# Optimization experiments

Measured on AMD Instinct MI355X. Metric: run time of the kernel, lower is better.

The kernel has to match this reference:

```python
import jax, jax.numpy as jnp
import numpy as np

N, MEM_SIZE, MEM_DIM = 65536, 2048, 256

def setup_inputs() -> dict:
    key = jax.random.key(0)
    k1, k2 = jax.random.split(key)
    x = jax.random.normal(k1, (N, MEM_DIM), dtype=jnp.float32)
    # xavier_uniform for memory parameter [memory_size, memory_dim]
    limit = np.sqrt(6.0 / (MEM_SIZE + MEM_DIM)).astype(np.float32)
    memory = jax.random.uniform(k2, (MEM_SIZE, MEM_DIM), dtype=jnp.float32,
                                minval=-limit, maxval=limit)
    return {"x": x, "memory": memory}

def reference(x, memory):
    # scores: [N, memory_size] = x @ memory^T (unscaled)
    scores = jnp.einsum('nd,md->nm', x, memory)
    attention_weights = jax.nn.softmax(scores, axis=-1)
    memory_output = jnp.einsum('nm,md->nd', attention_weights, memory)
    return (memory_output, attention_weights)
```

## Files before the change

kernel.cpp:

```cpp
#include <hip/hip_runtime.h>
#include <hip/hip_bf16.h>
#include <stdint.h>

#define NQ 65536
#define MM 2048
#define DD 256

typedef __bf16 bf16x8 __attribute__((ext_vector_type(8)));
typedef float f32x16 __attribute__((ext_vector_type(16)));
typedef unsigned short u16;
typedef unsigned int u32;
typedef u16 u16x8 __attribute__((ext_vector_type(8)));

typedef __attribute__((address_space(3))) u32 lds_u32;
typedef __attribute__((address_space(1))) u32 glb_u32;

#define GLOAD16(gsrc, ldst)                                                    \
  __builtin_amdgcn_global_load_lds((glb_u32*)(uintptr_t)(gsrc),                \
                                   (lds_u32*)(u32)(uintptr_t)(ldst), 16, 0, 0)

__device__ __forceinline__ u16 f32_to_bf16_rtne(float v) {
  u32 u = __builtin_bit_cast(u32, v);
  u += 0x7FFFu + ((u >> 16) & 1u);
  return (u16)(u >> 16);
}

__global__ __launch_bounds__(256) void mem_convert_kernel(
    const float* __restrict__ memory, u16* __restrict__ memb,
    u16* __restrict__ memTswz) {
  int tid = blockIdx.x * 256 + threadIdx.x;
  u16 b = f32_to_bf16_rtne(memory[tid]);
  memb[tid] = b;
  int m = tid >> 8, d = tid & 255;
  int t = m >> 5, mi = m & 31;
  int c = mi >> 3, e = mi & 7;
  int slot = c ^ ((d >> 1) & 3);
  memTswz[(size_t)t * 8192 + (size_t)(d * 4 + slot) * 8 + e] = b;
}


__global__ __launch_bounds__(256, 2) void pass1_kernel(
    const float* __restrict__ x, const u16* __restrict__ memb,
    u16* __restrict__ p_e, float* __restrict__ sums) {
  __shared__ __align__(16) char stage[2][32768];
  __shared__ __align__(16) u16 plds[4][32][40];

  const int tid = threadIdx.x;
  const int wv = tid >> 6;
  const int l = tid & 63;
  const int q5 = l & 31;
  const int h = l >> 5;
  const int qw = blockIdx.x * 128 + wv * 32;
  const int qt = blockIdx.x * 4 + wv;

  bf16x8 aq[16];
  {
    const float* xrow = x + (size_t)(qw + q5) * DD;
#pragma unroll
    for (int ks = 0; ks < 16; ++ks) {
      const float4 f0 = *(const float4*)(xrow + ks * 16 + h * 8);
      const float4 f1 = *(const float4*)(xrow + ks * 16 + h * 8 + 4);
      bf16x8 a;
      a[0] = (__bf16)f0.x; a[1] = (__bf16)f0.y;
      a[2] = (__bf16)f0.z; a[3] = (__bf16)f0.w;
      a[4] = (__bf16)f1.x; a[5] = (__bf16)f1.y;
      a[6] = (__bf16)f1.z; a[7] = (__bf16)f1.w;
      aq[ks] = a;
    }
  }

  auto STAGE1 = [&](int mt, char* buf) {
#pragma unroll
    for (int i = 0; i < 8; ++i) {
      const int wc = wv * 8 + i;
      const int row = wc * 2 + h;
      const int csrc = q5 ^ (row & 7);
      GLOAD16(memb + (((size_t)(mt * 64 + row)) << 8) + csrc * 8,
              buf + (wc << 10));
    }
  };

  float part[16];
#pragma unroll
  for (int r = 0; r < 16; ++r) part[r] = 0.f;

  STAGE1(0, stage[0]);
  __syncthreads();
  for (int mt = 0; mt < 32; ++mt) {
    char* cur = stage[mt & 1];
    char* nxt = stage[(mt & 1) ^ 1];
    if (mt + 1 < 32) STAGE1(mt + 1, nxt);
#pragma unroll
    for (int msub = 0; msub < 2; ++msub) {
      const int mrow = msub * 32 + q5;
      const char* bbase = cur + mrow * 512;
      const int sw = mrow & 7;
      f32x16 acc = 0.f;
      __builtin_amdgcn_s_setprio(1);
#pragma unroll
      for (int ks = 0; ks < 16; ++ks) {
        bf16x8 b = *(const bf16x8*)(bbase + (((ks * 2 + h) ^ sw) << 4));
        acc = __builtin_amdgcn_mfma_f32_32x32x16_bf16(aq[ks], b, acc, 0, 0, 0);
      }
      __builtin_amdgcn_s_setprio(0);
#pragma unroll
      for (int r = 0; r < 16; ++r) {
        const int qrow = (r & 3) + 8 * (r >> 2) + 4 * h;
        const float e = __expf(acc[r]);
        part[r] += e;
        plds[wv][qrow][q5] = f32_to_bf16_rtne(e);
      }
      asm volatile("s_waitcnt lgkmcnt(0)" ::: "memory");
      __builtin_amdgcn_sched_barrier(0);
      const int tm = mt * 2 + msub;
      u16* ptile = p_e + ((size_t)qt * 64 + tm) * 1024;
#pragma unroll
      for (int ks2 = 0; ks2 < 2; ++ks2) {
        const u16x8 pa = *(const u16x8*)&plds[wv][q5][ks2 * 16 + h * 8];
        *(u16x8*)(ptile + q5 * 32 + ks2 * 16 + h * 8) = pa;
      }
    }
    __syncthreads();
  }

#pragma unroll
  for (int r = 0; r < 16; ++r) {
    float p = part[r];
    p += __shfl_xor(p, 1, 64);
    p += __shfl_xor(p, 2, 64);
    p += __shfl_xor(p, 4, 64);
    p += __shfl_xor(p, 8, 64);
    p += __shfl_xor(p, 16, 64);
    if (q5 == 0) sums[qw + (r & 3) + 8 * (r >> 2) + 4 * h] = p;
  }
}

__global__ __launch_bounds__(256, 2) void pass2_kernel(
    const u16* __restrict__ p_e, const u16* __restrict__ memTswz,
    const float* __restrict__ sums, float* __restrict__ outO,
    float* __restrict__ outW) {
  __shared__ __align__(16) char tstage[2][32768];

  const int tid = threadIdx.x;
  const int wv = tid >> 6;
  const int l = tid & 63;
  const int q5 = l & 31;
  const int h = l >> 5;
  const int qw = blockIdx.x * 128 + wv * 32;
  const int qt = blockIdx.x * 4 + wv;

  const float inv_lane = 1.0f / sums[qw + q5];
  float invr[16];
#pragma unroll
  for (int r = 0; r < 16; ++r) {
    invr[r] = __shfl(inv_lane, (r & 3) + 8 * (r >> 2) + 4 * h, 64);
  }

  auto STAGE2T = [&](int pr, char* buf) {
#pragma unroll
    for (int i = 0; i < 8; ++i) {
      const int ci = wv * 8 + i;
      GLOAD16(memTswz + ((size_t)pr * 2048 + ci * 64 + l) * 8,
              buf + (ci << 10));
    }
  };

  const u16* pbase = p_e + (size_t)qt * 64 * 1024 + q5 * 32 + h * 8;
  u16x8 pec[4], pen[4];
#pragma unroll
  for (int j = 0; j < 4; ++j) {
    pec[j] = *(const u16x8*)(pbase + (size_t)(j >> 1) * 1024 + (j & 1) * 16);
  }

  f32x16 oacc[8];
#pragma unroll
  for (int i = 0; i < 8; ++i) oacc[i] = 0.f;

  STAGE2T(0, tstage[0]);
  __syncthreads();
  for (int pr = 0; pr < 32; ++pr) {
    char* cur = tstage[pr & 1];
    char* nxt = tstage[(pr & 1) ^ 1];
    if (pr + 1 < 32) {
      STAGE2T(pr + 1, nxt);
      const u16* pnext = pbase + (size_t)(pr + 1) * 2048;
#pragma unroll
      for (int j = 0; j < 4; ++j) {
        pen[j] =
            *(const u16x8*)(pnext + (size_t)(j >> 1) * 1024 + (j & 1) * 16);
      }
    }

#pragma unroll
    for (int tmi = 0; tmi < 2; ++tmi) {
      const char* ct = cur + tmi * 16384;
#pragma unroll
      for (int ks2 = 0; ks2 < 2; ++ks2) {
        const u16x8 pe = pec[tmi * 2 + ks2];
        float w[8];
#pragma unroll
        for (int j = 0; j < 8; ++j) {
          w[j] = __builtin_bit_cast(float, (u32)pe[j] << 16) * inv_lane;
        }
        float* base = outW + (size_t)(qw + q5) * MM + (pr * 2 + tmi) * 32 +
                      ks2 * 16 + h * 8;
        *(float4*)base = make_float4(w[0], w[1], w[2], w[3]);
        *(float4*)(base + 4) = make_float4(w[4], w[5], w[6], w[7]);
      }
      __builtin_amdgcn_s_setprio(1);
#pragma unroll
      for (int ks2 = 0; ks2 < 2; ++ks2) {
        const bf16x8 pa = __builtin_bit_cast(bf16x8, pec[tmi * 2 + ks2]);
#pragma unroll
        for (int dsub = 0; dsub < 8; ++dsub) {
          const int d = dsub * 32 + q5;
          const int slot = (2 * ks2 + h) ^ ((d >> 1) & 3);
          bf16x8 b = *(const bf16x8*)(ct + d * 64 + slot * 16);
          oacc[dsub] = __builtin_amdgcn_mfma_f32_32x32x16_bf16(pa, b,
                                                               oacc[dsub], 0,
                                                               0, 0);
        }
      }
      __builtin_amdgcn_s_setprio(0);
    }
    __syncthreads();
#pragma unroll
    for (int j = 0; j < 4; ++j) pec[j] = pen[j];
  }

#pragma unroll
  for (int dsub = 0; dsub < 8; ++dsub) {
#pragma unroll
    for (int r = 0; r < 16; ++r) {
      const int qrow = (r & 3) + 8 * (r >> 2) + 4 * h;
      outO[(size_t)(qw + qrow) * DD + dsub * 32 + q5] = oacc[dsub][r] * invr[r];
    }
  }
}

__global__ __launch_bounds__(256, 2) void pass1_fb(
    const float* __restrict__ x, const u16* __restrict__ memb,
    float* __restrict__ outWf, float* __restrict__ sums) {
  __shared__ __align__(16) char stage[2][32768];
  const int tid = threadIdx.x;
  const int wv = tid >> 6;
  const int l = tid & 63;
  const int q5 = l & 31;
  const int h = l >> 5;
  const int qw = blockIdx.x * 128 + wv * 32;

  bf16x8 aq[16];
  {
    const float* xrow = x + (size_t)(qw + q5) * DD;
#pragma unroll
    for (int ks = 0; ks < 16; ++ks) {
      const float4 f0 = *(const float4*)(xrow + ks * 16 + h * 8);
      const float4 f1 = *(const float4*)(xrow + ks * 16 + h * 8 + 4);
      bf16x8 a;
      a[0] = (__bf16)f0.x; a[1] = (__bf16)f0.y;
      a[2] = (__bf16)f0.z; a[3] = (__bf16)f0.w;
      a[4] = (__bf16)f1.x; a[5] = (__bf16)f1.y;
      a[6] = (__bf16)f1.z; a[7] = (__bf16)f1.w;
      aq[ks] = a;
    }
  }
  auto STAGE1 = [&](int mt, char* buf) {
#pragma unroll
    for (int i = 0; i < 8; ++i) {
      const int wc = wv * 8 + i;
      const int row = wc * 2 + h;
      const int csrc = q5 ^ (row & 7);
      GLOAD16(memb + (((size_t)(mt * 64 + row)) << 8) + csrc * 8,
              buf + (wc << 10));
    }
  };
  float part[16];
#pragma unroll
  for (int r = 0; r < 16; ++r) part[r] = 0.f;
  STAGE1(0, stage[0]);
  __syncthreads();
  for (int mt = 0; mt < 32; ++mt) {
    char* cur = stage[mt & 1];
    char* nxt = stage[(mt & 1) ^ 1];
    if (mt + 1 < 32) STAGE1(mt + 1, nxt);
#pragma unroll
    for (int msub = 0; msub < 2; ++msub) {
      const int mrow = msub * 32 + q5;
      const char* bbase = cur + mrow * 512;
      const int sw = mrow & 7;
      f32x16 acc = 0.f;
#pragma unroll
      for (int ks = 0; ks < 16; ++ks) {
        bf16x8 b = *(const bf16x8*)(bbase + (((ks * 2 + h) ^ sw) << 4));
        acc = __builtin_amdgcn_mfma_f32_32x32x16_bf16(aq[ks], b, acc, 0, 0, 0);
      }
      const int tm = mt * 2 + msub;
#pragma unroll
      for (int r = 0; r < 16; ++r) {
        const int qrow = (r & 3) + 8 * (r >> 2) + 4 * h;
        const float e = __expf(acc[r]);
        part[r] += e;
        outWf[(size_t)(qw + qrow) * MM + tm * 32 + q5] = e;
      }
    }
    __syncthreads();
  }
#pragma unroll
  for (int r = 0; r < 16; ++r) {
    float s = part[r];
    s += __shfl_xor(s, 1, 64);
    s += __shfl_xor(s, 2, 64);
    s += __shfl_xor(s, 4, 64);
    s += __shfl_xor(s, 8, 64);
    s += __shfl_xor(s, 16, 64);
    if (q5 == 0) sums[qw + (r & 3) + 8 * (r >> 2) + 4 * h] = s;
  }
}

__global__ __launch_bounds__(256, 2) void pass2_fb(
    const u16* __restrict__ memTswz, const float* __restrict__ sums,
    float* __restrict__ outO, float* __restrict__ outW) {
  __shared__ __align__(16) char tstage[2][16384];
  const int tid = threadIdx.x;
  const int wv = tid >> 6;
  const int l = tid & 63;
  const int q5 = l & 31;
  const int h = l >> 5;
  const int qw = blockIdx.x * 128 + wv * 32;
  const float inv_lane = 1.0f / sums[qw + q5];
  auto STAGE = [&](int t, char* buf) {
#pragma unroll
    for (int i = 0; i < 4; ++i) {
      const int ci = wv * 4 + i;
      GLOAD16(memTswz + ((size_t)t * 1024 + ci * 64 + l) * 8, buf + (ci << 10));
    }
  };
  f32x16 oacc[8];
#pragma unroll
  for (int i = 0; i < 8; ++i) oacc[i] = 0.f;
  STAGE(0, tstage[0]);
  __syncthreads();
  for (int tm = 0; tm < 64; ++tm) {
    char* cur = tstage[tm & 1];
    char* nxt = tstage[(tm & 1) ^ 1];
    if (tm + 1 < 64) STAGE(tm + 1, nxt);
    float* wrow = outW + (size_t)(qw + q5) * MM + tm * 32;
    bf16x8 pa[2];
#pragma unroll
    for (int ks2 = 0; ks2 < 2; ++ks2) {
      float4 f0 = *(const float4*)(wrow + ks2 * 16 + h * 8);
      float4 f1 = *(const float4*)(wrow + ks2 * 16 + h * 8 + 4);
      float w0 = f0.x * inv_lane, w1 = f0.y * inv_lane;
      float w2 = f0.z * inv_lane, w3 = f0.w * inv_lane;
      float w4 = f1.x * inv_lane, w5 = f1.y * inv_lane;
      float w6 = f1.z * inv_lane, w7 = f1.w * inv_lane;
      *(float4*)(wrow + ks2 * 16 + h * 8) = make_float4(w0, w1, w2, w3);
      *(float4*)(wrow + ks2 * 16 + h * 8 + 4) = make_float4(w4, w5, w6, w7);
      bf16x8 p;
      p[0] = (__bf16)w0; p[1] = (__bf16)w1; p[2] = (__bf16)w2;
      p[3] = (__bf16)w3; p[4] = (__bf16)w4; p[5] = (__bf16)w5;
      p[6] = (__bf16)w6; p[7] = (__bf16)w7;
      pa[ks2] = p;
    }
#pragma unroll
    for (int ks2 = 0; ks2 < 2; ++ks2) {
#pragma unroll
      for (int dsub = 0; dsub < 8; ++dsub) {
        const int d = dsub * 32 + q5;
        const int slot = (2 * ks2 + h) ^ ((d >> 1) & 3);
        bf16x8 b = *(const bf16x8*)(cur + d * 64 + slot * 16);
        oacc[dsub] =
            __builtin_amdgcn_mfma_f32_32x32x16_bf16(pa[ks2], b, oacc[dsub], 0,
                                                    0, 0);
      }
    }
    __syncthreads();
  }
#pragma unroll
  for (int dsub = 0; dsub < 8; ++dsub) {
#pragma unroll
    for (int r = 0; r < 16; ++r) {
      const int qrow = (r & 3) + 8 * (r >> 2) + 4 * h;
      outO[(size_t)(qw + qrow) * DD + dsub * 32 + q5] = oacc[dsub][r];
    }
  }
}

extern "C" void kernel_launch(void* const* d_in, const int* in_sizes, int n_in,
                              void* d_out, int out_size, void* d_ws,
                              size_t ws_size, hipStream_t stream) {
  const float* x = (const float*)d_in[0];
  const float* memory = (const float*)d_in[1];
  float* outO = (float*)d_out;
  float* outW = outO + (size_t)NQ * DD;

  u16* memb = (u16*)d_ws;
  u16* memTswz = memb + (size_t)MM * DD;
  float* sums = (float*)(memTswz + (size_t)MM * DD);
  u16* p_e = (u16*)(sums + NQ);
  const size_t need = (size_t)MM * DD * 2 * 2 + (size_t)NQ * 4 +
                      (size_t)NQ * MM * 2;

  mem_convert_kernel<<<dim3((MM * DD) / 256), dim3(256), 0, stream>>>(
      memory, memb, memTswz);
  if (ws_size >= need) {
    pass1_kernel<<<dim3(NQ / 128), dim3(256), 0, stream>>>(x, memb, p_e, sums);
    pass2_kernel<<<dim3(NQ / 128), dim3(256), 0, stream>>>(p_e, memTswz, sums,
                                                           outO, outW);
  } else {
    pass1_fb<<<dim3(NQ / 128), dim3(256), 0, stream>>>(x, memb, outW, sums);
    pass2_fb<<<dim3(NQ / 128), dim3(256), 0, stream>>>(memTswz, sums, outO,
                                                       outW);
  }
}
```

Baseline: 364.8 us.

## Split pass2 output dimension across wave pairs with 512-thread blocks

Pass2 now runs 8 waves per block. Each pair of waves shares a 32-query tile and splits the 256-wide output dimension in half, so each wave holds 4 accumulators instead of 8 and writes half of the weight stores. This lowers register pressure so launch bounds can request 4 blocks per SM, giving more occupancy to hide the bandwidth-heavy weight writes and p_e reads. In exchange, the software prefetch of the next p_e tile into registers is dropped and each wave reloads p_e every iteration, and p_e reads are duplicated across the wave pair.

Measured after the change: 735.4 us. 102% more time.

```diff
diff --git a/kernel.cpp b/kernel.cpp
--- a/kernel.cpp
+++ b/kernel.cpp
@@ -135,7 +135,7 @@
   }
 }
 
-__global__ __launch_bounds__(256, 2) void pass2_kernel(
+__global__ __launch_bounds__(512, 4) void pass2_kernel(
     const u16* __restrict__ p_e, const u16* __restrict__ memTswz,
     const float* __restrict__ sums, float* __restrict__ outO,
     float* __restrict__ outW) {
@@ -143,67 +143,57 @@
 
   const int tid = threadIdx.x;
   const int wv = tid >> 6;
+  const int qg = wv >> 1;
+  const int dh = wv & 1;
   const int l = tid & 63;
   const int q5 = l & 31;
   const int h = l >> 5;
-  const int qw = blockIdx.x * 128 + wv * 32;
-  const int qt = blockIdx.x * 4 + wv;
+  const int qw = blockIdx.x * 128 + qg * 32;
+  const int qt = blockIdx.x * 4 + qg;
 
   const float inv_lane = 1.0f / sums[qw + q5];
-  float invr[16];
-#pragma unroll
-  for (int r = 0; r < 16; ++r) {
-    invr[r] = __shfl(inv_lane, (r & 3) + 8 * (r >> 2) + 4 * h, 64);
-  }
 
   auto STAGE2T = [&](int pr, char* buf) {
 #pragma unroll
-    for (int i = 0; i < 8; ++i) {
-      const int ci = wv * 8 + i;
+    for (int i = 0; i < 4; ++i) {
+      const int ci = wv * 4 + i;
       GLOAD16(memTswz + ((size_t)pr * 2048 + ci * 64 + l) * 8,
               buf + (ci << 10));
     }
   };
 
   const u16* pbase = p_e + (size_t)qt * 64 * 1024 + q5 * 32 + h * 8;
-  u16x8 pec[4], pen[4];
-#pragma unroll
-  for (int j = 0; j < 4; ++j) {
-    pec[j] = *(const u16x8*)(pbase + (size_t)(j >> 1) * 1024 + (j & 1) * 16);
-  }
-
-  f32x16 oacc[8];
-#pragma unroll
-  for (int i = 0; i < 8; ++i) oacc[i] = 0.f;
+
+  f32x16 oacc[4];
+#pragma unroll
+  for (int i = 0; i < 4; ++i) oacc[i] = 0.f;
 
   STAGE2T(0, tstage[0]);
   __syncthreads();
   for (int pr = 0; pr < 32; ++pr) {
     char* cur = tstage[pr & 1];
     char* nxt = tstage[(pr & 1) ^ 1];
-    if (pr + 1 < 32) {
-      STAGE2T(pr + 1, nxt);
-      const u16* pnext = pbase + (size_t)(pr + 1) * 2048;
-#pragma unroll
-      for (int j = 0; j < 4; ++j) {
-        pen[j] =
-            *(const u16x8*)(pnext + (size_t)(j >> 1) * 1024 + (j & 1) * 16);
-      }
-    }
+
+    u16x8 pec[4];
+    const u16* pcur = pbase + (size_t)pr * 2048;
+#pragma unroll
+    for (int j = 0; j < 4; ++j) {
+      pec[j] = *(const u16x8*)(pcur + (size_t)(j >> 1) * 1024 + (j & 1) * 16);
+    }
+    if (pr + 1 < 32) STAGE2T(pr + 1, nxt);
 
 #pragma unroll
     for (int tmi = 0; tmi < 2; ++tmi) {
       const char* ct = cur + tmi * 16384;
-#pragma unroll
-      for (int ks2 = 0; ks2 < 2; ++ks2) {
-        const u16x8 pe = pec[tmi * 2 + ks2];
+      {
+        const u16x8 pe = pec[tmi * 2 + dh];
         float w[8];
 #pragma unroll
         for (int j = 0; j < 8; ++j) {
           w[j] = __builtin_bit_cast(float, (u32)pe[j] << 16) * inv_lane;
         }
         float* base = outW + (size_t)(qw + q5) * MM + (pr * 2 + tmi) * 32 +
-                      ks2 * 16 + h * 8;
+                      dh * 16 + h * 8;
         *(float4*)base = make_float4(w[0], w[1], w[2], w[3]);
         *(float4*)(base + 4) = make_float4(w[4], w[5], w[6], w[7]);
       }
@@ -212,28 +202,31 @@
       for (int ks2 = 0; ks2 < 2; ++ks2) {
         const bf16x8 pa = __builtin_bit_cast(bf16x8, pec[tmi * 2 + ks2]);
 #pragma unroll
-        for (int dsub = 0; dsub < 8; ++dsub) {
-          const int d = dsub * 32 + q5;
+        for (int i = 0; i < 4; ++i) {
+          const int d = (dh * 4 + i) * 32 + q5;
           const int slot = (2 * ks2 + h) ^ ((d >> 1) & 3);
           bf16x8 b = *(const bf16x8*)(ct + d * 64 + slot * 16);
-          oacc[dsub] = __builtin_amdgcn_mfma_f32_32x32x16_bf16(pa, b,
-                                                               oacc[dsub], 0,
-                                                               0, 0);
+          oacc[i] = __builtin_amdgcn_mfma_f32_32x32x16_bf16(pa, b, oacc[i], 0,
+                                                            0, 0);
         }
       }
       __builtin_amdgcn_s_setprio(0);
     }
     __syncthreads();
-#pragma unroll
-    for (int j = 0; j < 4; ++j) pec[j] = pen[j];
-  }
-
-#pragma unroll
-  for (int dsub = 0; dsub < 8; ++dsub) {
+  }
+
+  float invr[16];
+#pragma unroll
+  for (int r = 0; r < 16; ++r) {
+    invr[r] = __shfl(inv_lane, (r & 3) + 8 * (r >> 2) + 4 * h, 64);
+  }
+#pragma unroll
+  for (int i = 0; i < 4; ++i) {
 #pragma unroll
     for (int r = 0; r < 16; ++r) {
       const int qrow = (r & 3) + 8 * (r >> 2) + 4 * h;
-      outO[(size_t)(qw + qrow) * DD + dsub * 32 + q5] = oacc[dsub][r] * invr[r];
+      outO[(size_t)(qw + qrow) * DD + (dh * 4 + i) * 32 + q5] =
+          oacc[i][r] * invr[r];
     }
   }
 }
@@ -405,7 +398,7 @@
       memory, memb, memTswz);
   if (ws_size >= need) {
     pass1_kernel<<<dim3(NQ / 128), dim3(256), 0, stream>>>(x, memb, p_e, sums);
-    pass2_kernel<<<dim3(NQ / 128), dim3(256), 0, stream>>>(p_e, memTswz, sums,
+    pass2_kernel<<<dim3(NQ / 128), dim3(512), 0, stream>>>(p_e, memTswz, sums,
                                                            outO, outW);
   } else {
     pass1_fb<<<dim3(NQ / 128), dim3(256), 0, stream>>>(x, memb, outW, sums);
```

## Prepack memory into MFMA fragment order and read it directly from global

Applied to the files above, without the earlier changes.

The conversion kernel now writes the bf16 memory matrix and its transpose in per-lane MFMA fragment order. Both passes then load B operands directly from global memory (served by L2/L1) instead of staging tiles through LDS with double buffering and block barriers. This removes LDS traffic, the staging loads and the __syncthreads, but exposes global load latency to the MFMA loop with no explicit prefetch. Pass2 also stops prefetching the next P tile.

Measured after the change: 628.9 us. +72.4%, slower.

```diff
diff --git a/kernel.cpp b/kernel.cpp
--- a/kernel.cpp
+++ b/kernel.cpp
@@ -25,7 +25,29 @@
   return (u16)(u >> 16);
 }
 
-__global__ __launch_bounds__(256) void mem_convert_kernel(
+__global__ __launch_bounds__(256) void mem_convert_main(
+    const float* __restrict__ memory, u16* __restrict__ membfrag,
+    u16* __restrict__ memTfrag) {
+  int tid = blockIdx.x * 256 + threadIdx.x;
+  u16 b = f32_to_bf16_rtne(memory[tid]);
+  int m = tid >> 8, d = tid & 255;
+  int tm = m >> 5;
+  {
+    int q5m = m & 31;
+    int ks = d >> 4, hq = (d >> 3) & 1, jq = d & 7;
+    int lq = hq * 32 + q5m;
+    membfrag[(size_t)(tm * 16 + ks) * 512 + lq * 8 + jq] = b;
+  }
+  {
+    int mi = m & 31;
+    int ks2 = mi >> 4, hp = (mi >> 3) & 1, jp = mi & 7;
+    int dsub = d >> 5, d5 = d & 31;
+    int lp = hp * 32 + d5;
+    memTfrag[(size_t)(tm * 16 + ks2 * 8 + dsub) * 512 + lp * 8 + jp] = b;
+  }
+}
+
+__global__ __launch_bounds__(256) void mem_convert_fb(
     const float* __restrict__ memory, u16* __restrict__ memb,
     u16* __restrict__ memTswz) {
   int tid = blockIdx.x * 256 + threadIdx.x;
@@ -40,9 +62,8 @@
 
 
 __global__ __launch_bounds__(256, 2) void pass1_kernel(
-    const float* __restrict__ x, const u16* __restrict__ memb,
+    const float* __restrict__ x, const u16* __restrict__ membfrag,
     u16* __restrict__ p_e, float* __restrict__ sums) {
-  __shared__ __align__(16) char stage[2][32768];
   __shared__ __align__(16) u16 plds[4][32][40];
 
   const int tid = threadIdx.x;
@@ -69,58 +90,36 @@
     }
   }
 
-  auto STAGE1 = [&](int mt, char* buf) {
-#pragma unroll
-    for (int i = 0; i < 8; ++i) {
-      const int wc = wv * 8 + i;
-      const int row = wc * 2 + h;
-      const int csrc = q5 ^ (row & 7);
-      GLOAD16(memb + (((size_t)(mt * 64 + row)) << 8) + csrc * 8,
-              buf + (wc << 10));
-    }
-  };
-
   float part[16];
 #pragma unroll
   for (int r = 0; r < 16; ++r) part[r] = 0.f;
 
-  STAGE1(0, stage[0]);
-  __syncthreads();
-  for (int mt = 0; mt < 32; ++mt) {
-    char* cur = stage[mt & 1];
-    char* nxt = stage[(mt & 1) ^ 1];
-    if (mt + 1 < 32) STAGE1(mt + 1, nxt);
-#pragma unroll
-    for (int msub = 0; msub < 2; ++msub) {
-      const int mrow = msub * 32 + q5;
-      const char* bbase = cur + mrow * 512;
-      const int sw = mrow & 7;
-      f32x16 acc = 0.f;
-      __builtin_amdgcn_s_setprio(1);
-#pragma unroll
-      for (int ks = 0; ks < 16; ++ks) {
-        bf16x8 b = *(const bf16x8*)(bbase + (((ks * 2 + h) ^ sw) << 4));
-        acc = __builtin_amdgcn_mfma_f32_32x32x16_bf16(aq[ks], b, acc, 0, 0, 0);
-      }
-      __builtin_amdgcn_s_setprio(0);
-#pragma unroll
-      for (int r = 0; r < 16; ++r) {
-        const int qrow = (r & 3) + 8 * (r >> 2) + 4 * h;
-        const float e = __expf(acc[r]);
-        part[r] += e;
-        plds[wv][qrow][q5] = f32_to_bf16_rtne(e);
-      }
-      asm volatile("s_waitcnt lgkmcnt(0)" ::: "memory");
-      __builtin_amdgcn_sched_barrier(0);
-      const int tm = mt * 2 + msub;
-      u16* ptile = p_e + ((size_t)qt * 64 + tm) * 1024;
-#pragma unroll
-      for (int ks2 = 0; ks2 < 2; ++ks2) {
-        const u16x8 pa = *(const u16x8*)&plds[wv][q5][ks2 * 16 + h * 8];
-        *(u16x8*)(ptile + q5 * 32 + ks2 * 16 + h * 8) = pa;
-      }
-    }
-    __syncthreads();
+  const u16* fb = membfrag + l * 8;
+  for (int tm = 0; tm < 64; ++tm) {
+    const u16* tbase = fb + (size_t)tm * 8192;
+    f32x16 acc = 0.f;
+    __builtin_amdgcn_s_setprio(1);
+#pragma unroll
+    for (int ks = 0; ks < 16; ++ks) {
+      bf16x8 b = *(const bf16x8*)(tbase + ks * 512);
+      acc = __builtin_amdgcn_mfma_f32_32x32x16_bf16(aq[ks], b, acc, 0, 0, 0);
+    }
+    __builtin_amdgcn_s_setprio(0);
+#pragma unroll
+    for (int r = 0; r < 16; ++r) {
+      const int qrow = (r & 3) + 8 * (r >> 2) + 4 * h;
+      const float e = __expf(acc[r]);
+      part[r] += e;
+      plds[wv][qrow][q5] = f32_to_bf16_rtne(e);
+    }
+    asm volatile("s_waitcnt lgkmcnt(0)" ::: "memory");
+    __builtin_amdgcn_sched_barrier(0);
+    u16* ptile = p_e + ((size_t)qt * 64 + tm) * 1024;
+#pragma unroll
+    for (int ks2 = 0; ks2 < 2; ++ks2) {
+      const u16x8 pa = *(const u16x8*)&plds[wv][q5][ks2 * 16 + h * 8];
+      *(u16x8*)(ptile + q5 * 32 + ks2 * 16 + h * 8) = pa;
+    }
   }
 
 #pragma unroll
@@ -136,11 +135,9 @@
 }
 
 __global__ __launch_bounds__(256, 2) void pass2_kernel(
-    const u16* __restrict__ p_e, const u16* __restrict__ memTswz,
+    const u16* __restrict__ p_e, const u16* __restrict__ memTfrag,
     const float* __restrict__ sums, float* __restrict__ outO,
     float* __restrict__ outW) {
-  __shared__ __align__(16) char tstage[2][32768];
-
   const int tid = threadIdx.x;
   const int wv = tid >> 6;
   const int l = tid & 63;
@@ -150,84 +147,53 @@
   const int qt = blockIdx.x * 4 + wv;
 
   const float inv_lane = 1.0f / sums[qw + q5];
+
+  const u16* pbase = p_e + (size_t)qt * 64 * 1024 + q5 * 32 + h * 8;
+  const u16* fb = memTfrag + l * 8;
+
+  f32x16 oacc[8];
+#pragma unroll
+  for (int i = 0; i < 8; ++i) oacc[i] = 0.f;
+
+  for (int tm = 0; tm < 64; ++tm) {
+    u16x8 pec[2];
+    const u16* pcur = pbase + (size_t)tm * 1024;
+    pec[0] = *(const u16x8*)pcur;
+    pec[1] = *(const u16x8*)(pcur + 16);
+
+#pragma unroll
+    for (int ks2 = 0; ks2 < 2; ++ks2) {
+      const u16x8 pe = pec[ks2];
+      float w[8];
+#pragma unroll
+      for (int j = 0; j < 8; ++j) {
+        w[j] = __builtin_bit_cast(float, (u32)pe[j] << 16) * inv_lane;
+      }
+      float* base = outW + (size_t)(qw + q5) * MM + tm * 32 + ks2 * 16 + h * 8;
+      *(float4*)base = make_float4(w[0], w[1], w[2], w[3]);
+      *(float4*)(base + 4) = make_float4(w[4], w[5], w[6], w[7]);
+    }
+
+    const u16* tbase = fb + (size_t)tm * 8192;
+    __builtin_amdgcn_s_setprio(1);
+#pragma unroll
+    for (int ks2 = 0; ks2 < 2; ++ks2) {
+      const bf16x8 pa = __builtin_bit_cast(bf16x8, pec[ks2]);
+#pragma unroll
+      for (int dsub = 0; dsub < 8; ++dsub) {
+        bf16x8 b = *(const bf16x8*)(tbase + (ks2 * 8 + dsub) * 512);
+        oacc[dsub] =
+            __builtin_amdgcn_mfma_f32_32x32x16_bf16(pa, b, oacc[dsub], 0, 0, 0);
+      }
+    }
+    __builtin_amdgcn_s_setprio(0);
+  }
+
   float invr[16];
 #pragma unroll
   for (int r = 0; r < 16; ++r) {
     invr[r] = __shfl(inv_lane, (r & 3) + 8 * (r >> 2) + 4 * h, 64);
   }
-
-  auto STAGE2T = [&](int pr, char* buf) {
-#pragma unroll
-    for (int i = 0; i < 8; ++i) {
-      const int ci = wv * 8 + i;
-      GLOAD16(memTswz + ((size_t)pr * 2048 + ci * 64 + l) * 8,
-              buf + (ci << 10));
-    }
-  };
-
-  const u16* pbase = p_e + (size_t)qt * 64 * 1024 + q5 * 32 + h * 8;
-  u16x8 pec[4], pen[4];
-#pragma unroll
-  for (int j = 0; j < 4; ++j) {
-    pec[j] = *(const u16x8*)(pbase + (size_t)(j >> 1) * 1024 + (j & 1) * 16);
-  }
-
-  f32x16 oacc[8];
-#pragma unroll
-  for (int i = 0; i < 8; ++i) oacc[i] = 0.f;
-
-  STAGE2T(0, tstage[0]);
-  __syncthreads();
-  for (int pr = 0; pr < 32; ++pr) {
-    char* cur = tstage[pr & 1];
-    char* nxt = tstage[(pr & 1) ^ 1];
-    if (pr + 1 < 32) {
-      STAGE2T(pr + 1, nxt);
-      const u16* pnext = pbase + (size_t)(pr + 1) * 2048;
-#pragma unroll
-      for (int j = 0; j < 4; ++j) {
-        pen[j] =
-            *(const u16x8*)(pnext + (size_t)(j >> 1) * 1024 + (j & 1) * 16);
-      }
-    }
-
-#pragma unroll
-    for (int tmi = 0; tmi < 2; ++tmi) {
-      const char* ct = cur + tmi * 16384;
-#pragma unroll
-      for (int ks2 = 0; ks2 < 2; ++ks2) {
-        const u16x8 pe = pec[tmi * 2 + ks2];
-        float w[8];
-#pragma unroll
-        for (int j = 0; j < 8; ++j) {
-          w[j] = __builtin_bit_cast(float, (u32)pe[j] << 16) * inv_lane;
-        }
-        float* base = outW + (size_t)(qw + q5) * MM + (pr * 2 + tmi) * 32 +
-                      ks2 * 16 + h * 8;
-        *(float4*)base = make_float4(w[0], w[1], w[2], w[3]);
-        *(float4*)(base + 4) = make_float4(w[4], w[5], w[6], w[7]);
-      }
-      __builtin_amdgcn_s_setprio(1);
-#pragma unroll
-      for (int ks2 = 0; ks2 < 2; ++ks2) {
-        const bf16x8 pa = __builtin_bit_cast(bf16x8, pec[tmi * 2 + ks2]);
-#pragma unroll
-        for (int dsub = 0; dsub < 8; ++dsub) {
-          const int d = dsub * 32 + q5;
-          const int slot = (2 * ks2 + h) ^ ((d >> 1) & 3);
-          bf16x8 b = *(const bf16x8*)(ct + d * 64 + slot * 16);
-          oacc[dsub] = __builtin_amdgcn_mfma_f32_32x32x16_bf16(pa, b,
-                                                               oacc[dsub], 0,
-                                                               0, 0);
-        }
-      }
-      __builtin_amdgcn_s_setprio(0);
-    }
-    __syncthreads();
-#pragma unroll
-    for (int j = 0; j < 4; ++j) pec[j] = pen[j];
-  }
-
 #pragma unroll
   for (int dsub = 0; dsub < 8; ++dsub) {
 #pragma unroll
@@ -394,22 +360,23 @@
   float* outO = (float*)d_out;
   float* outW = outO + (size_t)NQ * DD;
 
-  u16* memb = (u16*)d_ws;
-  u16* memTswz = memb + (size_t)MM * DD;
-  float* sums = (float*)(memTswz + (size_t)MM * DD);
+  u16* buf0 = (u16*)d_ws;
+  u16* buf1 = buf0 + (size_t)MM * DD;
+  float* sums = (float*)(buf1 + (size_t)MM * DD);
   u16* p_e = (u16*)(sums + NQ);
   const size_t need = (size_t)MM * DD * 2 * 2 + (size_t)NQ * 4 +
                       (size_t)NQ * MM * 2;
 
-  mem_convert_kernel<<<dim3((MM * DD) / 256), dim3(256), 0, stream>>>(
-      memory, memb, memTswz);
   if (ws_size >= need) {
-    pass1_kernel<<<dim3(NQ / 128), dim3(256), 0, stream>>>(x, memb, p_e, sums);
-    pass2_kernel<<<dim3(NQ / 128), dim3(256), 0, stream>>>(p_e, memTswz, sums,
+    mem_convert_main<<<dim3((MM * DD) / 256), dim3(256), 0, stream>>>(
+        memory, buf0, buf1);
+    pass1_kernel<<<dim3(NQ / 128), dim3(256), 0, stream>>>(x, buf0, p_e, sums);
+    pass2_kernel<<<dim3(NQ / 128), dim3(256), 0, stream>>>(p_e, buf1, sums,
                                                            outO, outW);
   } else {
-    pass1_fb<<<dim3(NQ / 128), dim3(256), 0, stream>>>(x, memb, outW, sums);
-    pass2_fb<<<dim3(NQ / 128), dim3(256), 0, stream>>>(memTswz, sums, outO,
-                                                       outW);
-  }
-}
+    mem_convert_fb<<<dim3((MM * DD) / 256), dim3(256), 0, stream>>>(
+        memory, buf0, buf1);
+    pass1_fb<<<dim3(NQ / 128), dim3(256), 0, stream>>>(x, buf0, outW, sums);
+    pass2_fb<<<dim3(NQ / 128), dim3(256), 0, stream>>>(buf1, sums, outO, outW);
+  }
+}
```
